# Performance work log

Measured on AMD Instinct MI355X. Metric: run time of the kernel, lower is better.

## Reference

```python
import jax, jax.numpy as jnp
import numpy as np

K = 3       # deformable kernel size
STRIDE = 2
PAD = 1


def conv2d(x, w, b, stride, pad):
    out = jax.lax.conv_general_dilated(
        x, w, (stride, stride), [(pad, pad), (pad, pad)],
        dimension_numbers=('NCHW', 'OIHW', 'NCHW'))
    return out + b[None, :, None, None]


def setup_inputs() -> dict:
    key = jax.random.key(0)
    ks = jax.random.split(key, 5)
    B, C, H, W, OC = 8, 64, 256, 256, 128
    x = jax.random.normal(ks[0], (B, C, H, W), jnp.float32)
    # offset conv: in_c -> 3*K*K, 3x3, stride 2, pad 1 (small weights ~ trained state)
    offset_w = jax.random.normal(ks[1], (3 * K * K, C, 3, 3), jnp.float32) * 0.05
    offset_b = jax.random.normal(ks[2], (3 * K * K,), jnp.float32) * 0.05
    # main deformable conv weight/bias
    weight = jax.random.normal(ks[3], (OC, C, K, K), jnp.float32) * (1.0 / np.sqrt(C * K * K))
    bias = jax.random.normal(ks[4], (OC,), jnp.float32) * 0.01
    return {'x': x, 'offset_w': offset_w, 'offset_b': offset_b, 'weight': weight, 'bias': bias}


def _bilinear_gather(img, py, px):
    # img: [C, H, W]; py/px: [K2, Ho, Wo] float sampling coords (zero padding outside)
    C, H, W = img.shape
    y0 = jnp.floor(py); x0 = jnp.floor(px)
    y1 = y0 + 1.0;      x1 = x0 + 1.0
    wy1 = py - y0; wy0 = 1.0 - wy1
    wx1 = px - x0; wx0 = 1.0 - wx1

    def corner(yc, xc, wgt):
        valid = (yc >= 0) & (yc <= H - 1) & (xc >= 0) & (xc <= W - 1)
        yi = jnp.clip(yc, 0, H - 1).astype(jnp.int32)
        xi = jnp.clip(xc, 0, W - 1).astype(jnp.int32)
        v = img[:, yi, xi]                      # [C, K2, Ho, Wo]
        return v * (wgt * valid)[None]

    return (corner(y0, x0, wy0 * wx0) + corner(y0, x1, wy0 * wx1)
            + corner(y1, x0, wy1 * wx0) + corner(y1, x1, wy1 * wx1))


def reference(x, offset_w, offset_b, weight, bias):
    B, C, H, W = x.shape
    K2 = K * K
    # offset/mask branch (zero-initialized conv in original; random here = trained state)
    om = conv2d(x, offset_w, offset_b, STRIDE, PAD)       # [B, 3*K2, Ho, Wo]
    off_x, off_y, mask = jnp.split(om, 3, axis=1)         # chunk order from source
    mask = jax.nn.sigmoid(mask)                           # [B, K2, Ho, Wo]
    Ho, Wo = off_x.shape[2], off_x.shape[3]
    # base sampling grid: p0 (output pixel * stride - pad) + kernel point offset + learned offset
    hy = (jnp.arange(Ho) * STRIDE - PAD).astype(jnp.float32)
    wx = (jnp.arange(Wo) * STRIDE - PAD).astype(jnp.float32)
    ky, kx = jnp.meshgrid(jnp.arange(K), jnp.arange(K), indexing='ij')
    ky = ky.reshape(K2).astype(jnp.float32)
    kx = kx.reshape(K2).astype(jnp.float32)
    py = off_y + ky[None, :, None, None] + hy[None, None, :, None]  # [B, K2, Ho, Wo]
    px = off_x + kx[None, :, None, None] + wx[None, None, None, :]
    # bilinear gather per batch element -> [B, C, K2, Ho, Wo]
    sampled = jax.vmap(_bilinear_gather)(x, py, px)
    sampled = sampled * mask[:, None]                     # mask modulation
    w = weight.reshape(weight.shape[0], C, K2)
    out = jnp.einsum('bckhw,ock->bohw', sampled, w) + bias[None, :, None, None]
    return out
```

## Files before the change

### kernel.cpp

```cpp
#include <hip/hip_runtime.h>

typedef unsigned short u16;
typedef __attribute__((ext_vector_type(8))) short bf16x8;
typedef __attribute__((ext_vector_type(8))) unsigned short u16x8;
typedef __attribute__((ext_vector_type(4))) float f32x4;

#define HI 256
#define WI 256
#define CI 64
#define OC 128
#define HO 128
#define WO 128
#define NB 8
#define KC 576
#define KCP 584
#define TW 16

static __device__ __forceinline__ u16 f2bf(float f) {
    union { float f; unsigned u; } v; v.f = f;
    return (u16)((v.u + 0x7FFFu + ((v.u >> 16) & 1u)) >> 16);
}
static __device__ __forceinline__ float bf2f(u16 h) {
    union { unsigned u; float f; } v; v.u = ((unsigned)h) << 16;
    return v.f;
}

__global__ __launch_bounds__(256) void k_wconv(const float* __restrict__ w,
                                               const float* __restrict__ ow,
                                               u16* __restrict__ wbf, u16* __restrict__ wob) {
    int i = blockIdx.x * 256 + threadIdx.x;
    const int NW = OC * KCP;
    if (i < NW) {
        int oc = i / KCP, kc = i - oc * KCP;
        float v = (kc < KC) ? w[oc * KC + kc] : 0.f;
        wbf[i] = f2bf(v);
    } else {
        int i2 = i - NW;
        if (i2 < 32 * KCP) {
            int oc = i2 / KCP, kc = i2 - oc * KCP;
            float v = 0.f;
            if (oc < 27 && kc < KC) { int k = kc >> 6, c = kc & 63; v = ow[(oc * CI + c) * 9 + k]; }
            wob[i2] = f2bf(v);
        }
    }
}

__global__ __launch_bounds__(256) void k_tr(const float* __restrict__ x, u16* __restrict__ xT, int b0) {
    __shared__ u16 tile[64 * 68];
    const int t = threadIdx.x;
    const int w0 = blockIdx.x * 64;
    const int h  = blockIdx.y;
    const int bz = blockIdx.z;
    const float* xp = x + ((size_t)(b0 + bz) * CI) * (HI * WI) + h * WI + w0;
    #pragma unroll
    for (int i = 0; i < 4; ++i) {
        int c = i * 16 + (t >> 4);
        int w = (t & 15) * 4;
        float4 v = *(const float4*)(xp + (size_t)c * (HI * WI) + w);
        tile[(w + 0) * 68 + c] = f2bf(v.x);
        tile[(w + 1) * 68 + c] = f2bf(v.y);
        tile[(w + 2) * 68 + c] = f2bf(v.z);
        tile[(w + 3) * 68 + c] = f2bf(v.w);
    }
    __syncthreads();
    u16* op = xT + (size_t)bz * (HI * WI * CI) + ((size_t)h * WI + w0) * CI;
    #pragma unroll
    for (int j = 0; j < 4; ++j) {
        int w = j * 16 + (t >> 4);
        int c = (t & 15) * 4;
        *(ushort4*)(op + (size_t)w * CI + c) = *(const ushort4*)&tile[w * 68 + c];
    }
}

__global__ __launch_bounds__(256) void k_off(const u16* __restrict__ xT,
                                             const u16* __restrict__ wob,
                                             const float* __restrict__ ob,
                                             float* __restrict__ om) {
    __shared__ u16 s[32 * KCP];
    __shared__ int atab[288];
    __shared__ float red[2][2][64][4];
    const int t = threadIdx.x;
    const int wo0 = blockIdx.x * 32;
    const int ho = blockIdx.y;
    const int bz = blockIdx.z;
    const u16* xb = xT + (size_t)bz * (HI * WI * CI);

    for (int p = t; p < 288; p += 256) {
        int px = p / 9, k = p - px * 9;
        int ky = k / 3, kx = k - ky * 3;
        int y  = ho * 2 - 1 + ky;
        int xx = (wo0 + px) * 2 - 1 + kx;
        bool valid = ((unsigned)y < HI) && ((unsigned)xx < WI);
        atab[p] = valid ? (y * WI + xx) * CI : -1;
    }
    __syncthreads();

    #pragma unroll 3
    for (int it = 0; it < 9; ++it) {
        int idx = it * 256 + t;
        int p = idx >> 3, c8 = idx & 7;
        int a = atab[p];
        u16x8 v = {0, 0, 0, 0, 0, 0, 0, 0};
        if (a >= 0) v = *(const u16x8*)(xb + a + c8 * 8);
        int px = p / 9, k = p - px * 9;
        *(u16x8*)&s[px * KCP + k * 64 + c8 * 8] = v;
    }
    __syncthreads();

    const int lane = t & 63, wv = t >> 6;
    const int q = lane >> 4, l15 = lane & 15;
    const int ph = wv & 1, kh = wv >> 1;
    const u16* sp  = &s[(ph * 16 + l15) * KCP + kh * 288 + q * 8];
    const u16* wp0 = wob + l15 * KCP + kh * 288 + q * 8;
    const u16* wp1 = wob + (16 + l15) * KCP + kh * 288 + q * 8;
    f32x4 acc0 = {0.f, 0.f, 0.f, 0.f}, acc1 = {0.f, 0.f, 0.f, 0.f};
    #pragma unroll
    for (int kt = 0; kt < 9; ++kt) {
        bf16x8 a  = *(const bf16x8*)(sp  + kt * 32);
        bf16x8 b0 = *(const bf16x8*)(wp0 + kt * 32);
        bf16x8 b1 = *(const bf16x8*)(wp1 + kt * 32);
        acc0 = __builtin_amdgcn_mfma_f32_16x16x32_bf16(a, b0, acc0, 0, 0, 0);
        acc1 = __builtin_amdgcn_mfma_f32_16x16x32_bf16(a, b1, acc1, 0, 0, 0);
    }
    if (kh == 1) {
        #pragma unroll
        for (int r = 0; r < 4; ++r) { red[ph][0][lane][r] = acc0[r]; red[ph][1][lane][r] = acc1[r]; }
    }
    __syncthreads();
    if (kh == 0) {
        #pragma unroll
        for (int r = 0; r < 4; ++r) { acc0[r] += red[ph][0][lane][r]; acc1[r] += red[ph][1][lane][r]; }
        const int wo = wo0 + ph * 16 + q * 4;
        float bv0 = ob[l15];
        float* o0 = om + ((size_t)(bz * 27 + l15) * HO + ho) * WO + wo;
        *(float4*)o0 = make_float4(acc0[0] + bv0, acc0[1] + bv0, acc0[2] + bv0, acc0[3] + bv0);
        if (l15 < 11) {
            float bv1 = ob[16 + l15];
            float* o1 = om + ((size_t)(bz * 27 + 16 + l15) * HO + ho) * WO + wo;
            *(float4*)o1 = make_float4(acc1[0] + bv1, acc1[1] + bv1, acc1[2] + bv1, acc1[3] + bv1);
        }
    }
}

__global__ __launch_bounds__(256) void k_main(const u16* __restrict__ xT,
                                              const float* __restrict__ om,
                                              const u16* __restrict__ wbf,
                                              const float* __restrict__ bias,
                                              float* __restrict__ out, int b0) {
    __shared__ u16 s[TW * KCP];
    __shared__ int   la00[144], la01[144], la10[144], la11[144];
    __shared__ float lw00[144], lw01[144], lw10[144], lw11[144];

    const int t = threadIdx.x;
    const int wo0 = blockIdx.x * TW;
    const int ho = blockIdx.y;
    const int bz = blockIdx.z;
    const int b = b0 + bz;

    if (t < 144) {
        const int p = t;
        const int px_id = p / 9, k = p - px_id * 9;
        const int wo = wo0 + px_id;
        const size_t base = ((size_t)bz * 27) * (HO * WO) + ho * WO + wo;
        float oxv = om[base + (size_t)k * (HO * WO)];
        float oyv = om[base + (size_t)(9 + k) * (HO * WO)];
        float omm = om[base + (size_t)(18 + k) * (HO * WO)];
        float m = 1.f / (1.f + __expf(-omm));
        float py  = oyv + (float)(k / 3) + (float)(ho * 2 - 1);
        float pxf = oxv + (float)(k % 3) + (float)(wo * 2 - 1);
        float fy = floorf(py), fx = floorf(pxf);
        float wy1 = py - fy, wx1 = pxf - fx;
        float wy0 = 1.f - wy1, wx0 = 1.f - wx1;
        int y0 = (int)fy, x0i = (int)fx;
        int y1 = y0 + 1, x1i = x0i + 1;
        bool vy0 = (y0 >= 0) && (y0 < HI), vy1 = (y1 >= 0) && (y1 < HI);
        bool vx0 = (x0i >= 0) && (x0i < WI), vx1 = (x1i >= 0) && (x1i < WI);
        lw00[p] = (vy0 && vx0) ? wy0 * wx0 * m : 0.f;
        lw01[p] = (vy0 && vx1) ? wy0 * wx1 * m : 0.f;
        lw10[p] = (vy1 && vx0) ? wy1 * wx0 * m : 0.f;
        lw11[p] = (vy1 && vx1) ? wy1 * wx1 * m : 0.f;
        int y0c = (y0 < 0 ? 0 : (y0 > HI-1 ? HI-1 : y0));
        int y1c = (y1 < 0 ? 0 : (y1 > HI-1 ? HI-1 : y1));
        int x0c = (x0i < 0 ? 0 : (x0i > WI-1 ? WI-1 : x0i));
        int x1c = (x1i < 0 ? 0 : (x1i > WI-1 ? WI-1 : x1i));
        la00[p] = (y0c * WI + x0c) * CI;
        la01[p] = (y0c * WI + x1c) * CI;
        la10[p] = (y1c * WI + x0c) * CI;
        la11[p] = (y1c * WI + x1c) * CI;
    }
    __syncthreads();

    const u16* xb = xT + (size_t)bz * (HI * WI * CI);
    for (int i = t; i < 1152; i += 256) {
        int p = i >> 3;
        int co = (i & 7) * 8;
        int px_id = p / 9, k = p - px_id * 9;
        float w00 = lw00[p], w01 = lw01[p], w10 = lw10[p], w11 = lw11[p];
        u16x8 va = *(const u16x8*)(xb + la00[p] + co);
        u16x8 vb = *(const u16x8*)(xb + la01[p] + co);
        u16x8 vc = *(const u16x8*)(xb + la10[p] + co);
        u16x8 vd = *(const u16x8*)(xb + la11[p] + co);
        u16* sd = &s[px_id * KCP + k];
        #pragma unroll
        for (int j = 0; j < 8; ++j) {
            float v = w00 * bf2f(va[j]) + w01 * bf2f(vb[j])
                    + w10 * bf2f(vc[j]) + w11 * bf2f(vd[j]);
            sd[(co + j) * 9] = f2bf(v);
        }
    }
    __syncthreads();

    const int lane = t & 63, wv = t >> 6;
    const int q = lane >> 4, l15 = lane & 15;
    const u16* sp  = &s[l15 * KCP + q * 8];
    const int oc0 = wv * 32 + l15;
    const int oc1 = oc0 + 16;
    const u16* wp0 = wbf + oc0 * KCP + q * 8;
    const u16* wp1 = wbf + oc1 * KCP + q * 8;
    f32x4 acc0 = {0.f, 0.f, 0.f, 0.f};
    f32x4 acc1 = {0.f, 0.f, 0.f, 0.f};
    #pragma unroll
    for (int kt = 0; kt < 18; ++kt) {
        bf16x8 a  = *(const bf16x8*)(sp  + kt * 32);
        bf16x8 b0 = *(const bf16x8*)(wp0 + kt * 32);
        bf16x8 b1 = *(const bf16x8*)(wp1 + kt * 32);
        acc0 = __builtin_amdgcn_mfma_f32_16x16x32_bf16(a, b0, acc0, 0, 0, 0);
        acc1 = __builtin_amdgcn_mfma_f32_16x16x32_bf16(a, b1, acc1, 0, 0, 0);
    }
    const float bi0 = bias[oc0], bi1 = bias[oc1];
    const int px = q * 4;
    float* op0 = out + (((size_t)b * OC + oc0) * HO + ho) * WO + wo0 + px;
    float* op1 = out + (((size_t)b * OC + oc1) * HO + ho) * WO + wo0 + px;
    *(float4*)op0 = make_float4(acc0[0] + bi0, acc0[1] + bi0, acc0[2] + bi0, acc0[3] + bi0);
    *(float4*)op1 = make_float4(acc1[0] + bi1, acc1[1] + bi1, acc1[2] + bi1, acc1[3] + bi1);
}

extern "C" void kernel_launch(void* const* d_in, const int* in_sizes, int n_in,
                              void* d_out, int out_size, void* d_ws, size_t ws_size,
                              hipStream_t stream) {
    const float* x        = (const float*)d_in[0];
    const float* offset_w = (const float*)d_in[1];
    const float* offset_b = (const float*)d_in[2];
    const float* weight   = (const float*)d_in[3];
    const float* bias     = (const float*)d_in[4];
    float* out = (float*)d_out;

    const size_t xT_full = (size_t)NB * HI * WI * CI * 2;
    const size_t om_full = (size_t)NB * 27 * HO * WO * 4;
    const size_t xT_b    = (size_t)HI * WI * CI * 2;
    const size_t om_b    = (size_t)27 * HO * WO * 4;
    const size_t wsz     = (size_t)(OC + 32) * KCP * 2;
    const int nwb = (int)(((OC + 32) * KCP + 255) / 256);

    if (ws_size >= xT_full + om_full + wsz) {
        u16*   xT  = (u16*)d_ws;
        float* om  = (float*)((char*)d_ws + xT_full);
        u16*   wbf = (u16*)((char*)d_ws + xT_full + om_full);
        u16*   wob = wbf + OC * KCP;
        hipLaunchKernelGGL(k_wconv, dim3(nwb), dim3(256), 0, stream, weight, offset_w, wbf, wob);
        hipLaunchKernelGGL(k_tr,   dim3(4, 256, NB), dim3(256), 0, stream, x, xT, 0);
        hipLaunchKernelGGL(k_off,  dim3(4, 128, NB), dim3(256), 0, stream, xT, wob, offset_b, om);
        hipLaunchKernelGGL(k_main, dim3(8, 128, NB), dim3(256), 0, stream, xT, om, wbf, bias, out, 0);
    } else {
        u16*   xT  = (u16*)d_ws;
        float* om  = (float*)((char*)d_ws + xT_b);
        u16*   wbf = (u16*)((char*)d_ws + xT_b + om_b);
        u16*   wob = wbf + OC * KCP;
        hipLaunchKernelGGL(k_wconv, dim3(nwb), dim3(256), 0, stream, weight, offset_w, wbf, wob);
        for (int b = 0; b < NB; ++b) {
            hipLaunchKernelGGL(k_tr,   dim3(4, 256, 1), dim3(256), 0, stream, x, xT, b);
            hipLaunchKernelGGL(k_off,  dim3(4, 128, 1), dim3(256), 0, stream, xT, wob, offset_b, om);
            hipLaunchKernelGGL(k_main, dim3(8, 128, 1), dim3(256), 0, stream, xT, om, wbf, bias, out, b);
        }
    }
}
```

Measured before the change: 362.5 us.

## Reorder deformable K dimension to k-major, vectorize bilinear blend, swizzle workgroups

Reorders the reduction dimension of the main weight to k-major (k*64+c), matching the offset-conv layout. The sampled tile can then be written to LDS as one contiguous 16-byte store per thread instead of eight strided 2-byte stores. The bilinear blend now runs on packed f32x2 math with a hardware packed bf16 conversion, and the per-point address and weight tables are packed into int4/float4 LDS arrays. Both the offset and main kernels also remap workgroup IDs with an XCD-style swizzle (L&7 stride) so neighbouring tiles share L2 on the same die. The hardware conversion rounds slightly differently from the software f2bf, and the swizzle's index decode assumes the launch grid's exact dimensions.

```diff
diff --git a/kernel.cpp b/kernel.cpp
--- a/kernel.cpp
+++ b/kernel.cpp
@@ -4,6 +4,7 @@
 typedef __attribute__((ext_vector_type(8))) short bf16x8;
 typedef __attribute__((ext_vector_type(8))) unsigned short u16x8;
 typedef __attribute__((ext_vector_type(4))) float f32x4;
+typedef __attribute__((ext_vector_type(2))) float f32x2;
 
 #define HI 256
 #define WI 256
@@ -24,6 +25,13 @@
     union { unsigned u; float f; } v; v.u = ((unsigned)h) << 16;
     return v.f;
 }
+static __device__ __forceinline__ f32x2 unpack2(unsigned d) {
+    union { unsigned u; float f; } lo, hi;
+    lo.u = d << 16;
+    hi.u = d & 0xffff0000u;
+    f32x2 r; r.x = lo.f; r.y = hi.f;
+    return r;
+}
 
 __global__ __launch_bounds__(256) void k_wconv(const float* __restrict__ w,
                                                const float* __restrict__ ow,
@@ -32,7 +40,8 @@
     const int NW = OC * KCP;
     if (i < NW) {
         int oc = i / KCP, kc = i - oc * KCP;
-        float v = (kc < KC) ? w[oc * KC + kc] : 0.f;
+        float v = 0.f;
+        if (kc < KC) { int k = kc >> 6, c = kc & 63; v = w[oc * KC + c * 9 + k]; }
         wbf[i] = f2bf(v);
     } else {
         int i2 = i - NW;
@@ -80,9 +89,12 @@
     __shared__ int atab[288];
     __shared__ float red[2][2][64][4];
     const int t = threadIdx.x;
-    const int wo0 = blockIdx.x * 32;
-    const int ho = blockIdx.y;
-    const int bz = blockIdx.z;
+    const unsigned L = (blockIdx.z * gridDim.y + blockIdx.y) * gridDim.x + blockIdx.x;
+    const unsigned nwg = gridDim.x * gridDim.y * gridDim.z;
+    const unsigned W = (L & 7u) * (nwg >> 3) + (L >> 3);
+    const int wo0 = (W & 3u) * 32;
+    const int ho  = (W >> 2) & 127u;
+    const int bz  = W >> 9;
     const u16* xb = xT + (size_t)bz * (HI * WI * CI);
 
     for (int p = t; p < 288; p += 256) {
@@ -148,13 +160,16 @@
                                               const float* __restrict__ bias,
                                               float* __restrict__ out, int b0) {
     __shared__ u16 s[TW * KCP];
-    __shared__ int   la00[144], la01[144], la10[144], la11[144];
-    __shared__ float lw00[144], lw01[144], lw10[144], lw11[144];
+    __shared__ int4   lav[144];
+    __shared__ float4 lwv[144];
 
     const int t = threadIdx.x;
-    const int wo0 = blockIdx.x * TW;
-    const int ho = blockIdx.y;
-    const int bz = blockIdx.z;
+    const unsigned L = (blockIdx.z * gridDim.y + blockIdx.y) * gridDim.x + blockIdx.x;
+    const unsigned nwg = gridDim.x * gridDim.y * gridDim.z;
+    const unsigned W = (L & 7u) * (nwg >> 3) + (L >> 3);
+    const int wo0 = (W & 7u) * TW;
+    const int ho  = (W >> 3) & 127u;
+    const int bz  = W >> 10;
     const int b = b0 + bz;
 
     if (t < 144) {
@@ -175,18 +190,17 @@
         int y1 = y0 + 1, x1i = x0i + 1;
         bool vy0 = (y0 >= 0) && (y0 < HI), vy1 = (y1 >= 0) && (y1 < HI);
         bool vx0 = (x0i >= 0) && (x0i < WI), vx1 = (x1i >= 0) && (x1i < WI);
-        lw00[p] = (vy0 && vx0) ? wy0 * wx0 * m : 0.f;
-        lw01[p] = (vy0 && vx1) ? wy0 * wx1 * m : 0.f;
-        lw10[p] = (vy1 && vx0) ? wy1 * wx0 * m : 0.f;
-        lw11[p] = (vy1 && vx1) ? wy1 * wx1 * m : 0.f;
+        float w00 = (vy0 && vx0) ? wy0 * wx0 * m : 0.f;
+        float w01 = (vy0 && vx1) ? wy0 * wx1 * m : 0.f;
+        float w10 = (vy1 && vx0) ? wy1 * wx0 * m : 0.f;
+        float w11 = (vy1 && vx1) ? wy1 * wx1 * m : 0.f;
         int y0c = (y0 < 0 ? 0 : (y0 > HI-1 ? HI-1 : y0));
         int y1c = (y1 < 0 ? 0 : (y1 > HI-1 ? HI-1 : y1));
         int x0c = (x0i < 0 ? 0 : (x0i > WI-1 ? WI-1 : x0i));
         int x1c = (x1i < 0 ? 0 : (x1i > WI-1 ? WI-1 : x1i));
-        la00[p] = (y0c * WI + x0c) * CI;
-        la01[p] = (y0c * WI + x1c) * CI;
-        la10[p] = (y1c * WI + x0c) * CI;
-        la11[p] = (y1c * WI + x1c) * CI;
+        lwv[p] = make_float4(w00, w01, w10, w11);
+        lav[p] = make_int4((y0c * WI + x0c) * CI, (y0c * WI + x1c) * CI,
+                           (y1c * WI + x0c) * CI, (y1c * WI + x1c) * CI);
     }
     __syncthreads();
 
@@ -195,25 +209,35 @@
         int p = i >> 3;
         int co = (i & 7) * 8;
         int px_id = p / 9, k = p - px_id * 9;
-        float w00 = lw00[p], w01 = lw01[p], w10 = lw10[p], w11 = lw11[p];
-        u16x8 va = *(const u16x8*)(xb + la00[p] + co);
-        u16x8 vb = *(const u16x8*)(xb + la01[p] + co);
-        u16x8 vc = *(const u16x8*)(xb + la10[p] + co);
-        u16x8 vd = *(const u16x8*)(xb + la11[p] + co);
-        u16* sd = &s[px_id * KCP + k];
+        float4 wv = lwv[p];
+        int4   av = lav[p];
+        uint4 da = *(const uint4*)(xb + av.x + co);
+        uint4 db = *(const uint4*)(xb + av.y + co);
+        uint4 dc = *(const uint4*)(xb + av.z + co);
+        uint4 dd = *(const uint4*)(xb + av.w + co);
+        const unsigned* ua = (const unsigned*)&da;
+        const unsigned* ub = (const unsigned*)&db;
+        const unsigned* uc = (const unsigned*)&dc;
+        const unsigned* ud = (const unsigned*)&dd;
+        union { u16x8 v; unsigned u[4]; } r;
         #pragma unroll
-        for (int j = 0; j < 8; ++j) {
-            float v = w00 * bf2f(va[j]) + w01 * bf2f(vb[j])
-                    + w10 * bf2f(vc[j]) + w11 * bf2f(vd[j]);
-            sd[(co + j) * 9] = f2bf(v);
+        for (int j2 = 0; j2 < 4; ++j2) {
+            f32x2 e = wv.x * unpack2(ua[j2]);
+            e += wv.y * unpack2(ub[j2]);
+            e += wv.z * unpack2(uc[j2]);
+            e += wv.w * unpack2(ud[j2]);
+            unsigned pk;
+            asm("v_cvt_pk_bf16_f32 %0, %1, %2" : "=v"(pk) : "v"(e.x), "v"(e.y));
+            r.u[j2] = pk;
         }
-    }
-    __syncthreads();
-
-    const int lane = t & 63, wv = t >> 6;
+        *(u16x8*)&s[px_id * KCP + k * 64 + co] = r.v;
+    }
+    __syncthreads();
+
+    const int lane = t & 63, wv_ = t >> 6;
     const int q = lane >> 4, l15 = lane & 15;
     const u16* sp  = &s[l15 * KCP + q * 8];
-    const int oc0 = wv * 32 + l15;
+    const int oc0 = wv_ * 32 + l15;
     const int oc1 = oc0 + 16;
     const u16* wp0 = wbf + oc0 * KCP + q * 8;
     const u16* wp1 = wbf + oc1 * KCP + q * 8;
```

Measured after the change: 364.9 us. Within noise of the previous version (+0.7%).
